# Kernel tuning notes

Hardware: AMD Instinct MI355X
Metric: run time of the kernel (lower is better)

Reference implementation:

```python
import jax, jax.numpy as jnp
import numpy as np

P = 8        # patch (window) size
HEADS = 6
E = 192
HD = E // HEADS


def _layernorm(x, g, b, eps=1e-5):
    m = x.mean(-1, keepdims=True)
    v = ((x - m) ** 2).mean(-1, keepdims=True)
    return (x - m) / jnp.sqrt(v + eps) * g + b


def setup_inputs() -> dict:
    key = jax.random.key(0)
    ks = jax.random.split(key, 8)
    B, H, W = 8, 128, 128
    return {
        "x": jax.random.normal(ks[0], (B, E, H, W), jnp.float32),
        "row_embed": jax.random.uniform(ks[1], (P, E // 2), jnp.float32),
        "col_embed": jax.random.uniform(ks[2], (P, E // 2), jnp.float32),
        "ln1_g": jnp.ones((E,), jnp.float32),
        "ln1_b": jnp.zeros((E,), jnp.float32),
        "in_proj_w": jax.random.normal(ks[3], (3 * E, E), jnp.float32) * 0.02,
        "in_proj_b": jnp.zeros((3 * E,), jnp.float32),
        "out_w": jax.random.normal(ks[4], (E, E), jnp.float32) * 0.02,
        "out_b": jnp.zeros((E,), jnp.float32),
        "ln2_g": jnp.ones((E,), jnp.float32),
        "ln2_b": jnp.zeros((E,), jnp.float32),
        "ffn_w1": jax.random.normal(ks[5], (4 * E, E), jnp.float32) * 0.02,
        "ffn_b1": jnp.zeros((4 * E,), jnp.float32),
        "ffn_w2": jax.random.normal(ks[6], (E, 4 * E), jnp.float32) * 0.02,
        "ffn_b2": jnp.zeros((E,), jnp.float32),
    }


def reference(x, row_embed, col_embed, ln1_g, ln1_b, in_proj_w, in_proj_b,
              out_w, out_b, ln2_g, ln2_b, ffn_w1, ffn_b1, ffn_w2, ffn_b2):
    B, C, H, W = x.shape
    hp, wp = H // P, W // P
    # shift_size=0 and H,W multiples of P -> no roll, no padding, no mask.
    # to_patches: 'b c (hp p1) (wp p2) -> (p1 p2) (b hp wp) c'
    xp = (x.reshape(B, C, hp, P, wp, P)
           .transpose(3, 5, 0, 2, 4, 1)          # (p1, p2, B, hp, wp, C)
           .reshape(P * P, B * hp * wp, C))      # (L, N, C)
    # learnable positional embedding: (p^2, 1, E)
    pos = jnp.concatenate(
        [jnp.repeat(row_embed[:, None, :], P, axis=1),
         jnp.repeat(col_embed[None, :, :], P, axis=0)], axis=-1
    ).reshape(P * P, 1, C)
    xp = xp + pos
    residual = xp
    xn = _layernorm(xp, ln1_g, ln1_b)
    # self-attention (q = k = v = xn), torch MultiheadAttention math
    qkv = xn @ in_proj_w.T + in_proj_b            # (L, N, 3E)
    q, k, v = jnp.split(qkv, 3, axis=-1)
    L, N, _ = q.shape
    q = q.reshape(L, N, HEADS, HD)
    k = k.reshape(L, N, HEADS, HD)
    v = v.reshape(L, N, HEADS, HD)
    scale = 1.0 / jnp.sqrt(jnp.asarray(HD, jnp.float32))
    scores = jnp.einsum('lnhd,mnhd->nhlm', q * scale, k)   # (N, H, L, L)
    attn = jax.nn.softmax(scores, axis=-1)
    o = jnp.einsum('nhlm,mnhd->lnhd', attn, v).reshape(L, N, C)
    o = o @ out_w.T + out_b
    xp = o + residual
    # FFN (note: GELU after BOTH linears, per the source)
    h = _layernorm(xp, ln2_g, ln2_b)
    h = jax.nn.gelu(h @ ffn_w1.T + ffn_b1, approximate=False)
    h = jax.nn.gelu(h @ ffn_w2.T + ffn_b2, approximate=False)
    xp = xp + h
    # reverse rearrange: '(p1 p2) (b hp wp) c -> b c (hp p1) (wp p2)'
    out = (xp.reshape(P, P, B, hp, wp, C)
             .transpose(2, 5, 3, 0, 4, 1)        # (B, C, hp, p1, wp, p2)
             .reshape(B, C, H, W))
    return out
```

## Files before the change

### kernel.cpp

```cpp
#include <hip/hip_runtime.h>
#include <hip/hip_bf16.h>

typedef unsigned short u16;
typedef __bf16 bf16x8 __attribute__((ext_vector_type(8)));
typedef float f32x4 __attribute__((ext_vector_type(4)));

__device__ __forceinline__ u16 f2b(float f) {
  __hip_bfloat16 h = __float2bfloat16(f);
  return *reinterpret_cast<u16*>(&h);
}
__device__ __forceinline__ float b2f(u16 v) {
  unsigned int u = ((unsigned int)v) << 16;
  union { unsigned int u; float f; } c; c.u = u; return c.f;
}
__device__ __forceinline__ float gelu_f(float x) {
  float t = x * x;
  float u = x * fmaf(t, -0.10294576f, -2.30220813f);
  float e = exp2f(u);
  return x * __builtin_amdgcn_rcpf(1.0f + e);
}

__global__ __launch_bounds__(256) void k_cvt(const float* __restrict__ s, u16* __restrict__ d, int n) {
  int i = blockIdx.x * 256 + threadIdx.x;
  if (i < n) d[i] = f2b(s[i]);
}

__global__ __launch_bounds__(256) void k_patchify_ln(const float* __restrict__ x,
                                                     const float* __restrict__ rowe,
                                                     const float* __restrict__ cole,
                                                     const float* __restrict__ g,
                                                     const float* __restrict__ bta,
                                                     u16* __restrict__ resid,
                                                     u16* __restrict__ xn, int b0) {
  __shared__ float tile[192 * 133];
  __shared__ float ps[256], pq[256], mb[128], rb[128];
  const int h = blockIdx.x, bb = blockIdx.y, b = b0 + bb;
  const int tid = threadIdx.x;
  const int p1 = h & 7, hy = h >> 3;
  const float* xs = x + ((size_t)b * 192 * 128 + (size_t)h) * 128;
  for (int i = 0; i < 24; i++) {
    int idx = i * 256 + tid;
    int c = idx >> 5, w4 = idx & 31;
    const float4 v = *reinterpret_cast<const float4*>(xs + (size_t)c * 16384 + w4 * 4);
    float a0, a1, a2, a3;
    if (c < 96) {
      float pv = rowe[p1 * 96 + c];
      a0 = a1 = a2 = a3 = pv;
    } else {
      int w = w4 * 4;
      a0 = cole[((w)     & 7) * 96 + c - 96];
      a1 = cole[((w + 1) & 7) * 96 + c - 96];
      a2 = cole[((w + 2) & 7) * 96 + c - 96];
      a3 = cole[((w + 3) & 7) * 96 + c - 96];
    }
    float* t = &tile[c * 133 + w4 * 4];
    t[0] = v.x + a0; t[1] = v.y + a1; t[2] = v.z + a2; t[3] = v.w + a3;
  }
  __syncthreads();
  {
    int w = tid & 127, half = tid >> 7;
    float s = 0.f, q = 0.f;
    for (int c = half * 96; c < half * 96 + 96; c++) {
      float v = tile[c * 133 + w];
      s += v; q += v * v;
    }
    ps[tid] = s; pq[tid] = q;
  }
  __syncthreads();
  if (tid < 128) {
    float s = ps[tid] + ps[tid + 128];
    float q = pq[tid] + pq[tid + 128];
    float mean = s * (1.f / 192.f);
    float var = q * (1.f / 192.f) - mean * mean;
    mb[tid] = mean;
    rb[tid] = rsqrtf(var + 1e-5f);
  }
  __syncthreads();
  for (int i = 0; i < 96; i++) {
    int idx = i * 256 + tid;
    int w = idx / 192, c = idx - w * 192;
    float v = tile[c * 133 + w];
    int wx = w >> 3, p2 = w & 7;
    size_t rr = ((size_t)((bb * 16 + hy) * 16 + wx)) * 64 + p1 * 8 + p2;
    resid[rr * 192 + c] = f2b(v);
    xn[rr * 192 + c] = f2b((v - mb[w]) * rb[w] * g[c] + bta[c]);
  }
}

__global__ __launch_bounds__(256) void k_ln(const float* __restrict__ xin,
                                            const float* __restrict__ g,
                                            const float* __restrict__ bta,
                                            u16* __restrict__ outp) {
  const int wid = threadIdx.x >> 6, lane = threadIdx.x & 63;
  const size_t row = (size_t)blockIdx.x * 4 + wid;
  const float* p = xin + row * 192;
  float v0 = p[lane], v1 = p[lane + 64], v2 = p[lane + 128];
  float s = v0 + v1 + v2, q = v0 * v0 + v1 * v1 + v2 * v2;
  for (int m = 32; m >= 1; m >>= 1) { s += __shfl_xor(s, m, 64); q += __shfl_xor(q, m, 64); }
  float mean = s * (1.0f / 192.0f);
  float var = q * (1.0f / 192.0f) - mean * mean;
  float rstd = rsqrtf(var + 1e-5f);
  u16* o = outp + row * 192;
  o[lane]       = f2b((v0 - mean) * rstd * g[lane]       + bta[lane]);
  o[lane + 64]  = f2b((v1 - mean) * rstd * g[lane + 64]  + bta[lane + 64]);
  o[lane + 128] = f2b((v2 - mean) * rstd * g[lane + 128] + bta[lane + 128]);
}

enum { EP_BF16 = 0, EP_GELU_BF16 = 1, EP_RESID_F32 = 2, EP_GELU_ADD_F32 = 3 };

template <int BN, int EP, int KTOT>
__global__ __launch_bounds__(256, 2) void k_gemm3(const u16* __restrict__ A,
                                                  const u16* __restrict__ W,
                                                  const float* __restrict__ bias,
                                                  const void* __restrict__ aux,
                                                  void* __restrict__ outp, int Nout) {
  constexpr int NF = BN / 32;
  constexpr int NBS = BN / 32;
  constexpr int NK = KTOT / 64;
  __shared__ __align__(16) u16 ldsA[2][128 * 64];
  __shared__ __align__(16) u16 ldsB[2][BN * 64];
  const int tid = threadIdx.x;
  const int lane = tid & 63, wid = tid >> 6;
  const int lo = lane & 15, hi = lane >> 4;
  const int wm = wid >> 1, wn = wid & 1;
  const int n0 = blockIdx.x * BN;
  const int m0 = blockIdx.y * 128;

  const int lrow = lane >> 3, lk = (lane & 7) * 8;
  const u16* agp[4];
  const u16* bgp[NBS];
#pragma unroll
  for (int i = 0; i < 4; i++)
    agp[i] = A + (size_t)(m0 + i * 32 + wid * 8 + lrow) * KTOT + lk;
#pragma unroll
  for (int i = 0; i < NBS; i++)
    bgp[i] = W + (size_t)(n0 + i * 32 + wid * 8 + lrow) * KTOT + lk;

  auto stage = [&](int kc, int buf) {
#pragma unroll
    for (int i = 0; i < 4; i++)
      __builtin_amdgcn_global_load_lds(
          (const __attribute__((address_space(1))) void*)(agp[i] + kc * 64),
          (__attribute__((address_space(3))) void*)(&ldsA[buf][(i * 4 + wid) * 512]), 16, 0, 0);
#pragma unroll
    for (int i = 0; i < NBS; i++)
      __builtin_amdgcn_global_load_lds(
          (const __attribute__((address_space(1))) void*)(bgp[i] + kc * 64),
          (__attribute__((address_space(3))) void*)(&ldsB[buf][(i * 4 + wid) * 512]), 16, 0, 0);
  };

  f32x4 acc[4][NF] = {};
  stage(0, 0);
  __syncthreads();
  for (int kc = 0; kc < NK; kc++) {
    if (kc + 1 < NK) stage(kc + 1, (kc + 1) & 1);
    const u16* bufA = ldsA[kc & 1];
    const u16* bufB = ldsB[kc & 1];
#pragma unroll
    for (int kt = 0; kt < 2; kt++) {
      bf16x8 a[4], b[NF];
#pragma unroll
      for (int mi = 0; mi < 4; mi++)
        a[mi] = *reinterpret_cast<const bf16x8*>(&bufA[(wm * 64 + mi * 16 + lo) * 64 + kt * 32 + hi * 8]);
#pragma unroll
      for (int nj = 0; nj < NF; nj++)
        b[nj] = *reinterpret_cast<const bf16x8*>(&bufB[(wn * (BN / 2) + nj * 16 + lo) * 64 + kt * 32 + hi * 8]);
#pragma unroll
      for (int mi = 0; mi < 4; mi++)
#pragma unroll
        for (int nj = 0; nj < NF; nj++)
          acc[mi][nj] = __builtin_amdgcn_mfma_f32_16x16x32_bf16(a[mi], b[nj], acc[mi][nj], 0, 0, 0);
    }
    __syncthreads();
  }
#pragma unroll
  for (int mi = 0; mi < 4; mi++)
#pragma unroll
    for (int nj = 0; nj < NF; nj++) {
      int gn = n0 + wn * (BN / 2) + nj * 16 + lo;
      float bv = bias[gn];
#pragma unroll
      for (int r = 0; r < 4; r++) {
        int gm = m0 + wm * 64 + mi * 16 + hi * 4 + r;
        size_t oidx = (size_t)gm * Nout + gn;
        float v = acc[mi][nj][r] + bv;
        if (EP == EP_BF16)           ((u16*)outp)[oidx] = f2b(v);
        else if (EP == EP_GELU_BF16) ((u16*)outp)[oidx] = f2b(gelu_f(v));
        else if (EP == EP_RESID_F32) ((float*)outp)[oidx] = v + b2f(((const u16*)aux)[oidx]);
        else                         ((float*)outp)[oidx] = gelu_f(v) + ((const float*)aux)[oidx];
      }
    }
}

__global__ __launch_bounds__(384) void k_attn(const u16* __restrict__ qkv, u16* __restrict__ o) {
  __shared__ __align__(16) u16 qk_lds[64 * 392];
  __shared__ __align__(16) u16 vt[192 * 72];
  __shared__ __align__(16) u16 pbuf[6 * 64 * 72];
  const int tid = threadIdx.x;
  const u16* src = qkv + (size_t)blockIdx.x * 64 * 576;
  for (int i = 0; i < 8; i++) {
    int gq = i * 384 + tid, row = gq / 48, kk = gq % 48;
    uint4 d = *reinterpret_cast<const uint4*>(src + row * 576 + kk * 8);
    *reinterpret_cast<uint4*>(&qk_lds[row * 392 + kk * 8]) = d;
  }
  for (int i = 0; i < 4; i++) {
    int gq = i * 384 + tid, row = gq / 24, kk = gq % 24;
    uint4 d = *reinterpret_cast<const uint4*>(src + row * 576 + 384 + kk * 8);
    const u16* ds = reinterpret_cast<const u16*>(&d);
#pragma unroll
    for (int e = 0; e < 8; e++) vt[(kk * 8 + e) * 72 + row] = ds[e];
  }
  __syncthreads();
  const int wid = tid >> 6, lane = tid & 63, lo = lane & 15, hi = lane >> 4;
  f32x4 s[4][4] = {};
  const u16* pq = &qk_lds[lo * 392 + wid * 32 + hi * 8];
  const u16* pk = &qk_lds[lo * 392 + 192 + wid * 32 + hi * 8];
  bf16x8 qa[4], kb[4];
#pragma unroll
  for (int mi = 0; mi < 4; mi++) qa[mi] = *reinterpret_cast<const bf16x8*>(pq + mi * 16 * 392);
#pragma unroll
  for (int nj = 0; nj < 4; nj++) kb[nj] = *reinterpret_cast<const bf16x8*>(pk + nj * 16 * 392);
#pragma unroll
  for (int mi = 0; mi < 4; mi++)
#pragma unroll
    for (int nj = 0; nj < 4; nj++)
      s[mi][nj] = __builtin_amdgcn_mfma_f32_16x16x32_bf16(qa[mi], kb[nj], s[mi][nj], 0, 0, 0);
  const float scale = 0.1767766952966369f;
#pragma unroll
  for (int mi = 0; mi < 4; mi++)
#pragma unroll
    for (int nj = 0; nj < 4; nj++)
#pragma unroll
      for (int r = 0; r < 4; r++) s[mi][nj][r] *= scale;
#pragma unroll
  for (int mi = 0; mi < 4; mi++)
#pragma unroll
    for (int r = 0; r < 4; r++) {
      float mx = fmaxf(fmaxf(s[mi][0][r], s[mi][1][r]), fmaxf(s[mi][2][r], s[mi][3][r]));
      mx = fmaxf(mx, __shfl_xor(mx, 1, 64));
      mx = fmaxf(mx, __shfl_xor(mx, 2, 64));
      mx = fmaxf(mx, __shfl_xor(mx, 4, 64));
      mx = fmaxf(mx, __shfl_xor(mx, 8, 64));
      float e0 = __expf(s[mi][0][r] - mx), e1 = __expf(s[mi][1][r] - mx);
      float e2 = __expf(s[mi][2][r] - mx), e3 = __expf(s[mi][3][r] - mx);
      float sm = e0 + e1 + e2 + e3;
      sm += __shfl_xor(sm, 1, 64);
      sm += __shfl_xor(sm, 2, 64);
      sm += __shfl_xor(sm, 4, 64);
      sm += __shfl_xor(sm, 8, 64);
      float inv = 1.0f / sm;
      int i = mi * 16 + hi * 4 + r;
      u16* pr = &pbuf[wid * 4608 + i * 72 + lo];
      pr[0]  = f2b(e0 * inv);
      pr[16] = f2b(e1 * inv);
      pr[32] = f2b(e2 * inv);
      pr[48] = f2b(e3 * inv);
    }
  f32x4 oacc[4][2] = {};
  const u16* pp = &pbuf[wid * 4608 + lo * 72 + hi * 8];
  const u16* pv = &vt[(wid * 32 + lo) * 72 + hi * 8];
#pragma unroll
  for (int kt = 0; kt < 2; kt++) {
    bf16x8 pa[4], vb[2];
#pragma unroll
    for (int mi = 0; mi < 4; mi++) pa[mi] = *reinterpret_cast<const bf16x8*>(pp + mi * 16 * 72 + kt * 32);
#pragma unroll
    for (int ni = 0; ni < 2; ni++) vb[ni] = *reinterpret_cast<const bf16x8*>(pv + ni * 16 * 72 + kt * 32);
#pragma unroll
    for (int mi = 0; mi < 4; mi++)
#pragma unroll
      for (int ni = 0; ni < 2; ni++)
        oacc[mi][ni] = __builtin_amdgcn_mfma_f32_16x16x32_bf16(pa[mi], vb[ni], oacc[mi][ni], 0, 0, 0);
  }
#pragma unroll
  for (int mi = 0; mi < 4; mi++)
#pragma unroll
    for (int ni = 0; ni < 2; ni++)
#pragma unroll
      for (int r = 0; r < 4; r++) {
        int i = mi * 16 + hi * 4 + r, d = ni * 16 + lo;
        o[((size_t)blockIdx.x * 64 + i) * 192 + wid * 32 + d] = f2b(oacc[mi][ni][r]);
      }
}

__global__ __launch_bounds__(256) void k_unpatch(const float* __restrict__ xf, float* __restrict__ outp, int b0) {
  __shared__ float tile[128 * 65];
  const int cc = blockIdx.x, h = blockIdx.y, bb = blockIdx.z, b = b0 + bb;
  const int tid = threadIdx.x;
  const int p1 = h & 7, hy = h >> 3;
  for (int i = 0; i < 32; i++) {
    int idx = i * 256 + tid, t = idx >> 6, c = idx & 63;
    int wx = t >> 3, p2 = t & 7;
    int rr = ((bb * 16 + hy) * 16 + wx) * 64 + p1 * 8 + p2;
    tile[t * 65 + c] = xf[(size_t)rr * 192 + cc * 64 + c];
  }
  __syncthreads();
  for (int i = 0; i < 32; i++) {
    int idx = i * 256 + tid, c = idx >> 7, w = idx & 127;
    outp[((size_t)(b * 192 + cc * 64 + c) * 128 + h) * 128 + w] = tile[w * 65 + c];
  }
}

extern "C" void kernel_launch(void* const* d_in, const int* in_sizes, int n_in,
                              void* d_out, int out_size, void* d_ws, size_t ws_size,
                              hipStream_t stream) {
  const float* x    = (const float*)d_in[0];
  const float* rowe = (const float*)d_in[1];
  const float* cole = (const float*)d_in[2];
  const float* ln1g = (const float*)d_in[3];
  const float* ln1b = (const float*)d_in[4];
  const float* ipw  = (const float*)d_in[5];
  const float* ipb  = (const float*)d_in[6];
  const float* outw = (const float*)d_in[7];
  const float* outb = (const float*)d_in[8];
  const float* ln2g = (const float*)d_in[9];
  const float* ln2b = (const float*)d_in[10];
  const float* w1   = (const float*)d_in[11];
  const float* b1   = (const float*)d_in[12];
  const float* w2   = (const float*)d_in[13];
  const float* b2   = (const float*)d_in[14];
  float* outp = (float*)d_out;

  char* p = (char*)d_ws;
  auto alloc = [&](size_t bytes) -> void* {
    void* r = (void*)p;
    p += (bytes + 255) & ~(size_t)255;
    return r;
  };
  u16* wq  = (u16*)alloc(110592 * 2);
  u16* wo  = (u16*)alloc(36864 * 2);
  u16* wf1 = (u16*)alloc(147456 * 2);
  u16* wf2 = (u16*)alloc(147456 * 2);

  size_t used = (size_t)(p - (char*)d_ws);
  size_t avail = (ws_size > used) ? (ws_size - used) : 0;
  int NC = 1;
  while (NC < 8 && (size_t)(131072 / NC) * 4224 + 8192 > avail) NC *= 2;
  const int Bc = 8 / NC;
  const size_t Mc = (size_t)Bc * 16384;

  u16*   resid = (u16*)alloc(Mc * 192 * 2);
  u16*   xn    = (u16*)alloc(Mc * 192 * 2);
  u16*   big   = (u16*)alloc(Mc * 768 * 2);
  u16*   obuf  = (u16*)alloc(Mc * 192 * 2);
  float* xp2   = (float*)alloc(Mc * 192 * 4);
  float* xfin  = (float*)alloc(Mc * 192 * 4);

  k_cvt<<<dim3((110592 + 255) / 256), dim3(256), 0, stream>>>(ipw, wq, 110592);
  k_cvt<<<dim3((36864 + 255) / 256), dim3(256), 0, stream>>>(outw, wo, 36864);
  k_cvt<<<dim3((147456 + 255) / 256), dim3(256), 0, stream>>>(w1, wf1, 147456);
  k_cvt<<<dim3((147456 + 255) / 256), dim3(256), 0, stream>>>(w2, wf2, 147456);

  for (int ch = 0; ch < NC; ch++) {
    int b0 = ch * Bc;
    k_patchify_ln<<<dim3(128, Bc), dim3(256), 0, stream>>>(x, rowe, cole, ln1g, ln1b, resid, xn, b0);
    k_gemm3<96, EP_BF16, 192><<<dim3(6, (unsigned)(Mc / 128)), dim3(256), 0, stream>>>(xn, wq, ipb, nullptr, big, 576);
    k_attn<<<dim3((unsigned)(Bc * 256)), dim3(384), 0, stream>>>(big, obuf);
    k_gemm3<96, EP_RESID_F32, 192><<<dim3(2, (unsigned)(Mc / 128)), dim3(256), 0, stream>>>(obuf, wo, outb, resid, xp2, 192);
    k_ln<<<dim3((unsigned)(Mc / 4)), dim3(256), 0, stream>>>(xp2, ln2g, ln2b, xn);
    k_gemm3<128, EP_GELU_BF16, 192><<<dim3(6, (unsigned)(Mc / 128)), dim3(256), 0, stream>>>(xn, wf1, b1, nullptr, big, 768);
    k_gemm3<96, EP_GELU_ADD_F32, 768><<<dim3(2, (unsigned)(Mc / 128)), dim3(256), 0, stream>>>(big, wf2, b2, xp2, xfin, 192);
    k_unpatch<<<dim3(3, 128, Bc), dim3(256), 0, stream>>>(xfin, outp, b0);
  }
}
```

Baseline: 733.7 us.

## Replace LDS-staged GEMM with direct global-to-register MFMA loads and smaller M tiles

Drops the double-buffered LDS staging of A and W tiles and has each wave load its MFMA fragments straight from global memory into registers. The block M tile shrinks from 128 to 64 rows, doubling the grid, and occupancy hints are removed. The aim is to cut LDS traffic and barrier synchronisation for these short-K GEMMs, relying on L1/L2 caching of the reused weights. The cost is more redundant global loads across waves, with less latency hiding.

```diff
diff --git a/kernel.cpp b/kernel.cpp
--- a/kernel.cpp
+++ b/kernel.cpp
@@ -109,79 +109,49 @@
 enum { EP_BF16 = 0, EP_GELU_BF16 = 1, EP_RESID_F32 = 2, EP_GELU_ADD_F32 = 3 };
 
 template <int BN, int EP, int KTOT>
-__global__ __launch_bounds__(256, 2) void k_gemm3(const u16* __restrict__ A,
-                                                  const u16* __restrict__ W,
-                                                  const float* __restrict__ bias,
-                                                  const void* __restrict__ aux,
-                                                  void* __restrict__ outp, int Nout) {
+__global__ __launch_bounds__(256) void k_gemmd(const u16* __restrict__ A,
+                                               const u16* __restrict__ W,
+                                               const float* __restrict__ bias,
+                                               const void* __restrict__ aux,
+                                               void* __restrict__ outp, int Nout) {
   constexpr int NF = BN / 32;
-  constexpr int NBS = BN / 32;
-  constexpr int NK = KTOT / 64;
-  __shared__ __align__(16) u16 ldsA[2][128 * 64];
-  __shared__ __align__(16) u16 ldsB[2][BN * 64];
   const int tid = threadIdx.x;
   const int lane = tid & 63, wid = tid >> 6;
   const int lo = lane & 15, hi = lane >> 4;
   const int wm = wid >> 1, wn = wid & 1;
-  const int n0 = blockIdx.x * BN;
-  const int m0 = blockIdx.y * 128;
-
-  const int lrow = lane >> 3, lk = (lane & 7) * 8;
-  const u16* agp[4];
-  const u16* bgp[NBS];
-#pragma unroll
-  for (int i = 0; i < 4; i++)
-    agp[i] = A + (size_t)(m0 + i * 32 + wid * 8 + lrow) * KTOT + lk;
-#pragma unroll
-  for (int i = 0; i < NBS; i++)
-    bgp[i] = W + (size_t)(n0 + i * 32 + wid * 8 + lrow) * KTOT + lk;
-
-  auto stage = [&](int kc, int buf) {
-#pragma unroll
-    for (int i = 0; i < 4; i++)
-      __builtin_amdgcn_global_load_lds(
-          (const __attribute__((address_space(1))) void*)(agp[i] + kc * 64),
-          (__attribute__((address_space(3))) void*)(&ldsA[buf][(i * 4 + wid) * 512]), 16, 0, 0);
-#pragma unroll
-    for (int i = 0; i < NBS; i++)
-      __builtin_amdgcn_global_load_lds(
-          (const __attribute__((address_space(1))) void*)(bgp[i] + kc * 64),
-          (__attribute__((address_space(3))) void*)(&ldsB[buf][(i * 4 + wid) * 512]), 16, 0, 0);
-  };
-
-  f32x4 acc[4][NF] = {};
-  stage(0, 0);
-  __syncthreads();
-  for (int kc = 0; kc < NK; kc++) {
-    if (kc + 1 < NK) stage(kc + 1, (kc + 1) & 1);
-    const u16* bufA = ldsA[kc & 1];
-    const u16* bufB = ldsB[kc & 1];
-#pragma unroll
-    for (int kt = 0; kt < 2; kt++) {
-      bf16x8 a[4], b[NF];
-#pragma unroll
-      for (int mi = 0; mi < 4; mi++)
-        a[mi] = *reinterpret_cast<const bf16x8*>(&bufA[(wm * 64 + mi * 16 + lo) * 64 + kt * 32 + hi * 8]);
-#pragma unroll
-      for (int nj = 0; nj < NF; nj++)
-        b[nj] = *reinterpret_cast<const bf16x8*>(&bufB[(wn * (BN / 2) + nj * 16 + lo) * 64 + kt * 32 + hi * 8]);
-#pragma unroll
-      for (int mi = 0; mi < 4; mi++)
-#pragma unroll
-        for (int nj = 0; nj < NF; nj++)
-          acc[mi][nj] = __builtin_amdgcn_mfma_f32_16x16x32_bf16(a[mi], b[nj], acc[mi][nj], 0, 0, 0);
-    }
-    __syncthreads();
-  }
-#pragma unroll
-  for (int mi = 0; mi < 4; mi++)
+  const int m0 = blockIdx.y * 64 + wm * 32;
+  const int n0 = blockIdx.x * BN + wn * (BN / 2);
+  const u16* pa0 = A + (size_t)(m0 + lo) * KTOT + hi * 8;
+  const u16* pa1 = pa0 + (size_t)16 * KTOT;
+  const u16* pb[NF];
+#pragma unroll
+  for (int nj = 0; nj < NF; nj++)
+    pb[nj] = W + (size_t)(n0 + nj * 16 + lo) * KTOT + hi * 8;
+
+  f32x4 acc[2][NF] = {};
+#pragma unroll 6
+  for (int kt = 0; kt < KTOT / 32; kt++) {
+    bf16x8 a0 = *reinterpret_cast<const bf16x8*>(pa0 + kt * 32);
+    bf16x8 a1 = *reinterpret_cast<const bf16x8*>(pa1 + kt * 32);
+    bf16x8 b[NF];
+#pragma unroll
+    for (int nj = 0; nj < NF; nj++)
+      b[nj] = *reinterpret_cast<const bf16x8*>(pb[nj] + kt * 32);
 #pragma unroll
     for (int nj = 0; nj < NF; nj++) {
-      int gn = n0 + wn * (BN / 2) + nj * 16 + lo;
+      acc[0][nj] = __builtin_amdgcn_mfma_f32_16x16x32_bf16(a0, b[nj], acc[0][nj], 0, 0, 0);
+      acc[1][nj] = __builtin_amdgcn_mfma_f32_16x16x32_bf16(a1, b[nj], acc[1][nj], 0, 0, 0);
+    }
+  }
+#pragma unroll
+  for (int mi = 0; mi < 2; mi++)
+#pragma unroll
+    for (int nj = 0; nj < NF; nj++) {
+      int gn = n0 + nj * 16 + lo;
       float bv = bias[gn];
 #pragma unroll
       for (int r = 0; r < 4; r++) {
-        int gm = m0 + wm * 64 + mi * 16 + hi * 4 + r;
+        int gm = m0 + mi * 16 + hi * 4 + r;
         size_t oidx = (size_t)gm * Nout + gn;
         float v = acc[mi][nj][r] + bv;
         if (EP == EP_BF16)           ((u16*)outp)[oidx] = f2b(v);
@@ -354,12 +324,12 @@
   for (int ch = 0; ch < NC; ch++) {
     int b0 = ch * Bc;
     k_patchify_ln<<<dim3(128, Bc), dim3(256), 0, stream>>>(x, rowe, cole, ln1g, ln1b, resid, xn, b0);
-    k_gemm3<96, EP_BF16, 192><<<dim3(6, (unsigned)(Mc / 128)), dim3(256), 0, stream>>>(xn, wq, ipb, nullptr, big, 576);
+    k_gemmd<96, EP_BF16, 192><<<dim3(6, (unsigned)(Mc / 64)), dim3(256), 0, stream>>>(xn, wq, ipb, nullptr, big, 576);
     k_attn<<<dim3((unsigned)(Bc * 256)), dim3(384), 0, stream>>>(big, obuf);
-    k_gemm3<96, EP_RESID_F32, 192><<<dim3(2, (unsigned)(Mc / 128)), dim3(256), 0, stream>>>(obuf, wo, outb, resid, xp2, 192);
+    k_gemmd<96, EP_RESID_F32, 192><<<dim3(2, (unsigned)(Mc / 64)), dim3(256), 0, stream>>>(obuf, wo, outb, resid, xp2, 192);
     k_ln<<<dim3((unsigned)(Mc / 4)), dim3(256), 0, stream>>>(xp2, ln2g, ln2b, xn);
-    k_gemm3<128, EP_GELU_BF16, 192><<<dim3(6, (unsigned)(Mc / 128)), dim3(256), 0, stream>>>(xn, wf1, b1, nullptr, big, 768);
-    k_gemm3<96, EP_GELU_ADD_F32, 768><<<dim3(2, (unsigned)(Mc / 128)), dim3(256), 0, stream>>>(big, wf2, b2, xp2, xfin, 192);
+    k_gemmd<128, EP_GELU_BF16, 192><<<dim3(6, (unsigned)(Mc / 64)), dim3(256), 0, stream>>>(xn, wf1, b1, nullptr, big, 768);
+    k_gemmd<96, EP_GELU_ADD_F32, 768><<<dim3(2, (unsigned)(Mc / 64)), dim3(256), 0, stream>>>(big, wf2, b2, xp2, xfin, 192);
     k_unpatch<<<dim3(3, 128, Bc), dim3(256), 0, stream>>>(xfin, outp, b0);
   }
 }
```

Result: slower. 1.075 ms (+46.5%).

## Fuse output projection with LayerNorm, store residual in bf16, rework attention loads

Applied to the files above, without the earlier changes.

Adds a new out-projection GEMM with a full 192-wide tile. Its epilogue adds bias and residual, computes the LayerNorm2 statistics across waves through LDS, and writes both the bf16 residual stream and the normalized activations. This removes the separate LN kernel and the fp32 round trip of xp2. The attention kernel now loads Q and K straight from global memory into registers instead of staging them in LDS, and uses an XOR-swizzled P buffer to avoid bank conflicts. Keeping the intermediate residual in bf16 costs some precision.

```diff
diff --git a/kernel.cpp b/kernel.cpp
--- a/kernel.cpp
+++ b/kernel.cpp
@@ -87,26 +87,7 @@
   }
 }
 
-__global__ __launch_bounds__(256) void k_ln(const float* __restrict__ xin,
-                                            const float* __restrict__ g,
-                                            const float* __restrict__ bta,
-                                            u16* __restrict__ outp) {
-  const int wid = threadIdx.x >> 6, lane = threadIdx.x & 63;
-  const size_t row = (size_t)blockIdx.x * 4 + wid;
-  const float* p = xin + row * 192;
-  float v0 = p[lane], v1 = p[lane + 64], v2 = p[lane + 128];
-  float s = v0 + v1 + v2, q = v0 * v0 + v1 * v1 + v2 * v2;
-  for (int m = 32; m >= 1; m >>= 1) { s += __shfl_xor(s, m, 64); q += __shfl_xor(q, m, 64); }
-  float mean = s * (1.0f / 192.0f);
-  float var = q * (1.0f / 192.0f) - mean * mean;
-  float rstd = rsqrtf(var + 1e-5f);
-  u16* o = outp + row * 192;
-  o[lane]       = f2b((v0 - mean) * rstd * g[lane]       + bta[lane]);
-  o[lane + 64]  = f2b((v1 - mean) * rstd * g[lane + 64]  + bta[lane + 64]);
-  o[lane + 128] = f2b((v2 - mean) * rstd * g[lane + 128] + bta[lane + 128]);
-}
-
-enum { EP_BF16 = 0, EP_GELU_BF16 = 1, EP_RESID_F32 = 2, EP_GELU_ADD_F32 = 3 };
+enum { EP_BF16 = 0, EP_GELU_BF16 = 1, EP_GELU_ADD = 3 };
 
 template <int BN, int EP, int KTOT>
 __global__ __launch_bounds__(256, 2) void k_gemm3(const u16* __restrict__ A,
@@ -186,40 +167,138 @@
         float v = acc[mi][nj][r] + bv;
         if (EP == EP_BF16)           ((u16*)outp)[oidx] = f2b(v);
         else if (EP == EP_GELU_BF16) ((u16*)outp)[oidx] = f2b(gelu_f(v));
-        else if (EP == EP_RESID_F32) ((float*)outp)[oidx] = v + b2f(((const u16*)aux)[oidx]);
-        else                         ((float*)outp)[oidx] = gelu_f(v) + ((const float*)aux)[oidx];
+        else                         ((float*)outp)[oidx] = gelu_f(v) + b2f(((const u16*)aux)[oidx]);
       }
     }
 }
 
-__global__ __launch_bounds__(384) void k_attn(const u16* __restrict__ qkv, u16* __restrict__ o) {
-  __shared__ __align__(16) u16 qk_lds[64 * 392];
+__global__ __launch_bounds__(256, 2) void k_oproj_ln(const u16* __restrict__ A,
+                                                     const u16* __restrict__ W,
+                                                     const float* __restrict__ bias,
+                                                     const u16* __restrict__ resid,
+                                                     const float* __restrict__ g,
+                                                     const float* __restrict__ bt,
+                                                     u16* __restrict__ xp2,
+                                                     u16* __restrict__ xn) {
+  __shared__ __align__(16) u16 ldsA[2][128 * 64];
+  __shared__ __align__(16) u16 ldsB[2][192 * 64];
+  const int tid = threadIdx.x;
+  const int lane = tid & 63, wid = tid >> 6;
+  const int lo = lane & 15, hi = lane >> 4;
+  const int wm = wid >> 1, wn = wid & 1;
+  const size_t m0 = (size_t)blockIdx.x * 128;
+  const int lrow = lane >> 3, lk = (lane & 7) * 8;
+
+  auto stage = [&](int kc, int buf) {
+#pragma unroll
+    for (int i = 0; i < 4; i++)
+      __builtin_amdgcn_global_load_lds(
+          (const __attribute__((address_space(1))) void*)(A + (m0 + i * 32 + wid * 8 + lrow) * 192 + kc * 64 + lk),
+          (__attribute__((address_space(3))) void*)(&ldsA[buf][(i * 4 + wid) * 512]), 16, 0, 0);
+#pragma unroll
+    for (int i = 0; i < 6; i++)
+      __builtin_amdgcn_global_load_lds(
+          (const __attribute__((address_space(1))) void*)(W + (size_t)(i * 32 + wid * 8 + lrow) * 192 + kc * 64 + lk),
+          (__attribute__((address_space(3))) void*)(&ldsB[buf][(i * 4 + wid) * 512]), 16, 0, 0);
+  };
+
+  f32x4 acc[4][6] = {};
+  stage(0, 0);
+  __syncthreads();
+  for (int kc = 0; kc < 3; kc++) {
+    if (kc + 1 < 3) stage(kc + 1, (kc + 1) & 1);
+    const u16* bufA = ldsA[kc & 1];
+    const u16* bufB = ldsB[kc & 1];
+#pragma unroll
+    for (int kt = 0; kt < 2; kt++) {
+      bf16x8 a[4], b[6];
+#pragma unroll
+      for (int mi = 0; mi < 4; mi++)
+        a[mi] = *reinterpret_cast<const bf16x8*>(&bufA[(wm * 64 + mi * 16 + lo) * 64 + kt * 32 + hi * 8]);
+#pragma unroll
+      for (int nj = 0; nj < 6; nj++)
+        b[nj] = *reinterpret_cast<const bf16x8*>(&bufB[(wn * 96 + nj * 16 + lo) * 64 + kt * 32 + hi * 8]);
+#pragma unroll
+      for (int mi = 0; mi < 4; mi++)
+#pragma unroll
+        for (int nj = 0; nj < 6; nj++)
+          acc[mi][nj] = __builtin_amdgcn_mfma_f32_16x16x32_bf16(a[mi], b[nj], acc[mi][nj], 0, 0, 0);
+    }
+    __syncthreads();
+  }
+  float bv[6];
+#pragma unroll
+  for (int nj = 0; nj < 6; nj++) bv[nj] = bias[wn * 96 + nj * 16 + lo];
+#pragma unroll
+  for (int mi = 0; mi < 4; mi++)
+#pragma unroll
+    for (int r = 0; r < 4; r++) {
+      size_t gm = m0 + wm * 64 + mi * 16 + hi * 4 + r;
+#pragma unroll
+      for (int nj = 0; nj < 6; nj++)
+        acc[mi][nj][r] += bv[nj] + b2f(resid[gm * 192 + wn * 96 + nj * 16 + lo]);
+    }
+  float* scr_s = (float*)&ldsA[0][0];
+  float* scr_q = scr_s + 256;
+#pragma unroll
+  for (int mi = 0; mi < 4; mi++)
+#pragma unroll
+    for (int r = 0; r < 4; r++) {
+      float s = 0.f, q = 0.f;
+#pragma unroll
+      for (int nj = 0; nj < 6; nj++) { float v = acc[mi][nj][r]; s += v; q += v * v; }
+      s += __shfl_xor(s, 1, 64); q += __shfl_xor(q, 1, 64);
+      s += __shfl_xor(s, 2, 64); q += __shfl_xor(q, 2, 64);
+      s += __shfl_xor(s, 4, 64); q += __shfl_xor(q, 4, 64);
+      s += __shfl_xor(s, 8, 64); q += __shfl_xor(q, 8, 64);
+      if (lo == 0) {
+        int row = wm * 64 + mi * 16 + hi * 4 + r;
+        scr_s[row * 2 + wn] = s;
+        scr_q[row * 2 + wn] = q;
+      }
+    }
+  __syncthreads();
+#pragma unroll
+  for (int mi = 0; mi < 4; mi++)
+#pragma unroll
+    for (int r = 0; r < 4; r++) {
+      int row = wm * 64 + mi * 16 + hi * 4 + r;
+      float s = scr_s[row * 2] + scr_s[row * 2 + 1];
+      float q = scr_q[row * 2] + scr_q[row * 2 + 1];
+      float mean = s * (1.f / 192.f);
+      float rstd = rsqrtf(q * (1.f / 192.f) - mean * mean + 1e-5f);
+#pragma unroll
+      for (int nj = 0; nj < 6; nj++) {
+        int gn = wn * 96 + nj * 16 + lo;
+        size_t oidx = (m0 + row) * 192 + gn;
+        float v = acc[mi][nj][r];
+        xp2[oidx] = f2b(v);
+        xn[oidx] = f2b((v - mean) * rstd * g[gn] + bt[gn]);
+      }
+    }
+}
+
+__global__ __launch_bounds__(384, 3) void k_attn2(const u16* __restrict__ qkv, u16* __restrict__ o) {
   __shared__ __align__(16) u16 vt[192 * 72];
-  __shared__ __align__(16) u16 pbuf[6 * 64 * 72];
+  __shared__ __align__(16) u16 pbuf[6 * 64 * 64];
   const int tid = threadIdx.x;
+  const int wid = tid >> 6, lane = tid & 63, lo = lane & 15, hi = lane >> 4;
   const u16* src = qkv + (size_t)blockIdx.x * 64 * 576;
-  for (int i = 0; i < 8; i++) {
-    int gq = i * 384 + tid, row = gq / 48, kk = gq % 48;
-    uint4 d = *reinterpret_cast<const uint4*>(src + row * 576 + kk * 8);
-    *reinterpret_cast<uint4*>(&qk_lds[row * 392 + kk * 8]) = d;
-  }
   for (int i = 0; i < 4; i++) {
-    int gq = i * 384 + tid, row = gq / 24, kk = gq % 24;
+    int gq = i * 384 + tid, row = gq / 24, kk = gq - row * 24;
     uint4 d = *reinterpret_cast<const uint4*>(src + row * 576 + 384 + kk * 8);
-    const u16* ds = reinterpret_cast<const u16*>(&d);
+    const u16* ds = (const u16*)&d;
 #pragma unroll
     for (int e = 0; e < 8; e++) vt[(kk * 8 + e) * 72 + row] = ds[e];
   }
-  __syncthreads();
-  const int wid = tid >> 6, lane = tid & 63, lo = lane & 15, hi = lane >> 4;
+  bf16x8 qa[4], kb[4];
+#pragma unroll
+  for (int mi = 0; mi < 4; mi++)
+    qa[mi] = *reinterpret_cast<const bf16x8*>(src + (size_t)(mi * 16 + lo) * 576 + wid * 32 + hi * 8);
+#pragma unroll
+  for (int nj = 0; nj < 4; nj++)
+    kb[nj] = *reinterpret_cast<const bf16x8*>(src + (size_t)(nj * 16 + lo) * 576 + 192 + wid * 32 + hi * 8);
   f32x4 s[4][4] = {};
-  const u16* pq = &qk_lds[lo * 392 + wid * 32 + hi * 8];
-  const u16* pk = &qk_lds[lo * 392 + 192 + wid * 32 + hi * 8];
-  bf16x8 qa[4], kb[4];
-#pragma unroll
-  for (int mi = 0; mi < 4; mi++) qa[mi] = *reinterpret_cast<const bf16x8*>(pq + mi * 16 * 392);
-#pragma unroll
-  for (int nj = 0; nj < 4; nj++) kb[nj] = *reinterpret_cast<const bf16x8*>(pk + nj * 16 * 392);
 #pragma unroll
   for (int mi = 0; mi < 4; mi++)
 #pragma unroll
@@ -232,6 +311,7 @@
     for (int nj = 0; nj < 4; nj++)
 #pragma unroll
       for (int r = 0; r < 4; r++) s[mi][nj][r] *= scale;
+  const int l3 = lo & 7, lh = lo >> 3;
 #pragma unroll
   for (int mi = 0; mi < 4; mi++)
 #pragma unroll
@@ -249,23 +329,27 @@
       sm += __shfl_xor(sm, 4, 64);
       sm += __shfl_xor(sm, 8, 64);
       float inv = 1.0f / sm;
-      int i = mi * 16 + hi * 4 + r;
-      u16* pr = &pbuf[wid * 4608 + i * 72 + lo];
-      pr[0]  = f2b(e0 * inv);
-      pr[16] = f2b(e1 * inv);
-      pr[32] = f2b(e2 * inv);
-      pr[48] = f2b(e3 * inv);
-    }
+      int ii = mi * 16 + hi * 4 + r;
+      u16* bse = pbuf + wid * 4096 + ii * 64;
+      int x7 = ii & 7;
+      bse[((lh)     ^ x7) * 8 + l3] = f2b(e0 * inv);
+      bse[((2 + lh) ^ x7) * 8 + l3] = f2b(e1 * inv);
+      bse[((4 + lh) ^ x7) * 8 + l3] = f2b(e2 * inv);
+      bse[((6 + lh) ^ x7) * 8 + l3] = f2b(e3 * inv);
+    }
+  __syncthreads();
   f32x4 oacc[4][2] = {};
-  const u16* pp = &pbuf[wid * 4608 + lo * 72 + hi * 8];
-  const u16* pv = &vt[(wid * 32 + lo) * 72 + hi * 8];
 #pragma unroll
   for (int kt = 0; kt < 2; kt++) {
     bf16x8 pa[4], vb[2];
 #pragma unroll
-    for (int mi = 0; mi < 4; mi++) pa[mi] = *reinterpret_cast<const bf16x8*>(pp + mi * 16 * 72 + kt * 32);
-#pragma unroll
-    for (int ni = 0; ni < 2; ni++) vb[ni] = *reinterpret_cast<const bf16x8*>(pv + ni * 16 * 72 + kt * 32);
+    for (int mi = 0; mi < 4; mi++) {
+      int row = mi * 16 + lo;
+      pa[mi] = *reinterpret_cast<const bf16x8*>(pbuf + wid * 4096 + row * 64 + ((kt * 4 + hi) ^ (row & 7)) * 8);
+    }
+#pragma unroll
+    for (int ni = 0; ni < 2; ni++)
+      vb[ni] = *reinterpret_cast<const bf16x8*>(vt + (wid * 32 + ni * 16 + lo) * 72 + kt * 32 + hi * 8);
 #pragma unroll
     for (int mi = 0; mi < 4; mi++)
 #pragma unroll
@@ -335,7 +419,7 @@
   size_t used = (size_t)(p - (char*)d_ws);
   size_t avail = (ws_size > used) ? (ws_size - used) : 0;
   int NC = 1;
-  while (NC < 8 && (size_t)(131072 / NC) * 4224 + 8192 > avail) NC *= 2;
+  while (NC < 8 && (size_t)(131072 / NC) * 3840 + 8192 > avail) NC *= 2;
   const int Bc = 8 / NC;
   const size_t Mc = (size_t)Bc * 16384;
 
@@ -343,7 +427,7 @@
   u16*   xn    = (u16*)alloc(Mc * 192 * 2);
   u16*   big   = (u16*)alloc(Mc * 768 * 2);
   u16*   obuf  = (u16*)alloc(Mc * 192 * 2);
-  float* xp2   = (float*)alloc(Mc * 192 * 4);
+  u16*   xp2   = (u16*)alloc(Mc * 192 * 2);
   float* xfin  = (float*)alloc(Mc * 192 * 4);
 
   k_cvt<<<dim3((110592 + 255) / 256), dim3(256), 0, stream>>>(ipw, wq, 110592);
@@ -355,11 +439,10 @@
     int b0 = ch * Bc;
     k_patchify_ln<<<dim3(128, Bc), dim3(256), 0, stream>>>(x, rowe, cole, ln1g, ln1b, resid, xn, b0);
     k_gemm3<96, EP_BF16, 192><<<dim3(6, (unsigned)(Mc / 128)), dim3(256), 0, stream>>>(xn, wq, ipb, nullptr, big, 576);
-    k_attn<<<dim3((unsigned)(Bc * 256)), dim3(384), 0, stream>>>(big, obuf);
-    k_gemm3<96, EP_RESID_F32, 192><<<dim3(2, (unsigned)(Mc / 128)), dim3(256), 0, stream>>>(obuf, wo, outb, resid, xp2, 192);
-    k_ln<<<dim3((unsigned)(Mc / 4)), dim3(256), 0, stream>>>(xp2, ln2g, ln2b, xn);
+    k_attn2<<<dim3((unsigned)(Bc * 256)), dim3(384), 0, stream>>>(big, obuf);
+    k_oproj_ln<<<dim3((unsigned)(Mc / 128)), dim3(256), 0, stream>>>(obuf, wo, outb, resid, ln2g, ln2b, xp2, xn);
     k_gemm3<128, EP_GELU_BF16, 192><<<dim3(6, (unsigned)(Mc / 128)), dim3(256), 0, stream>>>(xn, wf1, b1, nullptr, big, 768);
-    k_gemm3<96, EP_GELU_ADD_F32, 768><<<dim3(2, (unsigned)(Mc / 128)), dim3(256), 0, stream>>>(big, wf2, b2, xp2, xfin, 192);
+    k_gemm3<96, EP_GELU_ADD, 768><<<dim3(2, (unsigned)(Mc / 128)), dim3(256), 0, stream>>>(big, wf2, b2, xp2, xfin, 192);
     k_unpatch<<<dim3(3, 128, Bc), dim3(256), 0, stream>>>(xfin, outp, b0);
   }
 }
```

Result: faster. 705.9 us (-3.8%).
